# Kernel tuning notes

Measured on AMD Instinct MI355X. Metric: run time of the kernel, lower is better.

Reference implementation:

```python
import jax, jax.numpy as jnp
import numpy as np

N = 128            # codeword length (power of 2)
LIST = 8           # SCL list size
L2 = 2 * LIST      # decoders kept during path expansion
STAGES = 7         # log2(N)
LLR_MAX = 30.0
BATCH = 2048
FROZEN_POS = np.arange(N // 2)
FROZEN_IND = np.zeros(N, dtype=bool)
FROZEN_IND[FROZEN_POS] = True
INFO_POS = np.setdiff1d(np.arange(N), FROZEN_POS)


def _cn_op(x, y):
    # min-sum boxplus with LLR clipping
    x = jnp.clip(x, -LLR_MAX, LLR_MAX)
    y = jnp.clip(y, -LLR_MAX, LLR_MAX)
    return jnp.sign(x) * jnp.sign(y) * jnp.minimum(jnp.abs(x), jnp.abs(y))


def _vn_op(x, y, u):
    return (1.0 - 2.0 * u) * x + y


def _leaf(state, i):
    # Update single bit i across all 2L decoders, update path metrics,
    # and for info bits sort + duplicate the best L paths.
    uhat, llr, pm, ptr, bidx = state
    frozen = bool(FROZEN_IND[i])
    if not frozen:
        # set bit=1 for the upper half of decoders (path expansion)
        u_slice = uhat[:, :, 0, i]
        u_slice = u_slice.at[bidx[:, None], ptr[:, LIST:]].set(1.0)
        uhat = uhat.at[:, :, 0, i].set(u_slice)
    # path metric update, Eq.(10) of Stimming et al.
    u = jnp.take_along_axis(uhat[:, :, 0, i], ptr, axis=1)
    l = jnp.clip(jnp.take_along_axis(llr[:, :, 0, i], ptr, axis=1), -LLR_MAX, LLR_MAX)
    pm = pm + jax.nn.softplus(-(1.0 - 2.0 * u) * l)
    if not frozen:
        order = jnp.argsort(pm, axis=-1)
        pm = jnp.take_along_axis(pm, order, axis=1)
        ptr = jnp.take_along_axis(ptr, order, axis=1)
        lo = ptr[:, :LIST]
        up = ptr[:, LIST:]
        uhat = uhat.at[bidx[:, None], up].set(uhat[bidx[:, None], lo])
        llr = llr.at[bidx[:, None], up].set(llr[bidx[:, None], lo])
        pm = pm.at[:, LIST:].set(pm[:, :LIST])
    return (uhat, llr, pm, ptr, bidx)


def _decode(state, start, length):
    # recursive SCL tree traversal over contiguous index block [start, start+length)
    if length == 1:
        return _leaf(state, start)
    s = int(np.log2(length))
    h = length // 2
    uhat, llr, pm, ptr, bidx = state
    lsl = slice(start, start + h)
    rsl = slice(start + h, start + length)
    # f (check-node) update -> left child
    f = _cn_op(llr[:, :, s, lsl], llr[:, :, s, rsl])
    llr = llr.at[:, :, s - 1, lsl].set(f)
    uhat, llr, pm, ptr, bidx = _decode((uhat, llr, pm, ptr, bidx), start, h)
    # g (variable-node) update -> right child
    g = _vn_op(llr[:, :, s, lsl], llr[:, :, s, rsl], uhat[:, :, s - 1, lsl])
    llr = llr.at[:, :, s - 1, rsl].set(g)
    uhat, llr, pm, ptr, bidx = _decode((uhat, llr, pm, ptr, bidx), start + h, h)
    # combine partial sums: left XOR right, right pass-through
    ul = uhat[:, :, s - 1, lsl]
    ur = uhat[:, :, s - 1, rsl]
    ux = ul + ur - 2.0 * ul * ur  # XOR for {0,1} values (differentiable form)
    uhat = uhat.at[:, :, s, start:start + length].set(jnp.concatenate([ux, ur], axis=-1))
    return (uhat, llr, pm, ptr, bidx)


def setup_inputs() -> dict:
    key = jax.random.key(0)
    inputs = 2.0 * jax.random.normal(key, (BATCH, N), dtype=jnp.float32)
    return {"inputs": inputs}


def reference(inputs):
    bs = inputs.shape[0]
    llr_ch = -inputs.astype(jnp.float32)  # logits -> LLR sign convention
    uhat = jnp.zeros((bs, L2, STAGES + 1, N), jnp.float32)
    llr = jnp.zeros((bs, L2, STAGES + 1, N), jnp.float32)
    llr = llr.at[:, :, STAGES, :].set(llr_ch[:, None, :])
    pm = jnp.zeros((bs, L2), jnp.float32)
    pm = pm.at[:, 1:LIST].set(LLR_MAX).at[:, LIST + 1:].set(LLR_MAX)
    ptr = jnp.tile(jnp.arange(L2)[None, :], (bs, 1))
    bidx = jnp.arange(bs)
    uhat, llr, pm, ptr, _ = _decode((uhat, llr, pm, ptr, bidx), 0, N)
    # final sort and de-permutation of the list dimension
    order = jnp.argsort(pm, axis=-1)
    pm = jnp.take_along_axis(pm, order, axis=1)
    ptr = jnp.take_along_axis(ptr, order, axis=1)
    uhat = uhat[bidx[:, None], ptr]
    cand = jnp.argmin(pm, axis=-1)
    c_hat = uhat[bidx, cand, 0, :]       # [bs, n] best codeword estimate
    return c_hat[:, INFO_POS]            # [bs, k] info bits
```

## Files before the change

### kernel.cpp

```cpp
#include <hip/hip_runtime.h>
#include <math.h>

#define LMAX 30.0f
typedef unsigned long long ull;
typedef unsigned int u32;

__device__ __forceinline__ float clip30(float x) { return fminf(fmaxf(x, -LMAX), LMAX); }
__device__ __forceinline__ float cnop(float x, float y) {
    x = clip30(x); y = clip30(y);
    const float m = fminf(fabsf(x), fabsf(y));
    const unsigned sg = (__float_as_uint(x) ^ __float_as_uint(y)) & 0x80000000u;
    return __uint_as_float(__float_as_uint(m) | sg);
}

#define SWZI(x, PAT) __builtin_amdgcn_ds_swizzle((x), (PAT))
#define SWZF(x, PAT) __int_as_float(__builtin_amdgcn_ds_swizzle(__float_as_int(x), (PAT)))

template<int CTRL>
__device__ __forceinline__ int dppi(int x) {
    return __builtin_amdgcn_update_dpp(x, x, CTRL, 0xF, 0xF, false);
}
template<int CTRL>
__device__ __forceinline__ float dppf(float x) {
    return __int_as_float(dppi<CTRL>(__float_as_int(x)));
}
#define CTL_XOR8 0x128
#define CTL_XOR2 0x4E
#define CTL_XOR1 0xB1

#if __has_builtin(__builtin_amdgcn_permlane16_swap)
typedef int v2j_ __attribute__((ext_vector_type(2)));
__device__ __forceinline__ int swap16i(int x) {
    v2j_ r = __builtin_amdgcn_permlane16_swap(x, x, false, false);
    return (r[0] != x) ? r[0] : r[1];
}
#else
__device__ __forceinline__ int swap16i(int x) { return SWZI(x, 0x401F); }
#endif
__device__ __forceinline__ float swap16f(float x) { return __int_as_float(swap16i(__float_as_int(x))); }

__device__ __forceinline__ float gfb(float v, int a) {
    return __int_as_float(__builtin_amdgcn_ds_bpermute(a, __float_as_int(v)));
}
__device__ __forceinline__ u32 gub(u32 v, int a) {
    return (u32)__builtin_amdgcn_ds_bpermute(a, (int)v);
}

__device__ __forceinline__ u32 enc2(u32 w)  { w ^= (w >> 1) & 0x1u; return w; }
__device__ __forceinline__ u32 enc4(u32 w)  { w ^= (w >> 1) & 0x5u; w ^= (w >> 2) & 0x3u; return w; }
__device__ __forceinline__ u32 enc8(u32 w)  { w ^= (w >> 1) & 0x55u; w ^= (w >> 2) & 0x33u;
                                              w ^= (w >> 4) & 0x0fu; return w; }
__device__ __forceinline__ u32 enc16(u32 w) { w ^= (w >> 1) & 0x5555u; w ^= (w >> 2) & 0x3333u;
                                              w ^= (w >> 4) & 0x0f0fu; w ^= (w >> 8) & 0x00ffu; return w; }
__device__ __forceinline__ u32 enc32(u32 w) { w ^= (w >> 1) & 0x55555555u; w ^= (w >> 2) & 0x33333333u;
                                              w ^= (w >> 4) & 0x0f0f0f0fu; w ^= (w >> 8) & 0x00ff00ffu;
                                              w ^= (w >> 16) & 0x0000ffffu; return w; }

struct Dec {
    float C[32];
    float S5[16], S4[8], S3[4], R2[4], R1[2];
    float pm;
    u32 uhPrev, uhCur;
    int rF;
    int q, pos, gbase, A0, idx0;
    u32 upB;
    bool isUp;
};

__device__ __forceinline__ void f6(Dec& s) {
    #pragma unroll
    for (int k = 0; k < 16; ++k) s.S5[k] = cnop(s.C[k], s.C[k + 16]);
}
__device__ __forceinline__ void g6p(Dec& s) {
    const u32 ub = enc32(s.uhPrev);
    #pragma unroll
    for (int k = 0; k < 16; ++k) {
        const int u = (ub >> (s.q + 2 * k)) & 1;
        s.S5[k] = u ? (s.C[k + 16] - s.C[k]) : (s.C[k + 16] + s.C[k]);
    }
}
__device__ __forceinline__ void f5(Dec& s) {
    #pragma unroll
    for (int k = 0; k < 8; ++k) s.S4[k] = cnop(s.S5[k], s.S5[k + 8]);
}
template<int L> __device__ __forceinline__ void g5l(Dec& s) {
    const u32 ub = enc16((s.uhCur >> (L - 16)) & 0xffffu);
    #pragma unroll
    for (int k = 0; k < 8; ++k) {
        const int u = (ub >> (s.q + 2 * k)) & 1;
        s.S4[k] = u ? (s.S5[k + 8] - s.S5[k]) : (s.S5[k + 8] + s.S5[k]);
    }
}
__device__ __forceinline__ void f4(Dec& s) {
    #pragma unroll
    for (int k = 0; k < 4; ++k) s.S3[k] = cnop(s.S4[k], s.S4[k + 4]);
}
template<int L> __device__ __forceinline__ void g4l(Dec& s) {
    const u32 ub = enc8((s.uhCur >> (L - 8)) & 0xffu);
    #pragma unroll
    for (int k = 0; k < 4; ++k) {
        const int u = (ub >> (s.q + 2 * k)) & 1;
        s.S3[k] = u ? (s.S4[k + 4] - s.S4[k]) : (s.S4[k + 4] + s.S4[k]);
    }
}
__device__ __forceinline__ void repl2(Dec& s, float t0, float t1) {
    const float P0 = swap16f(t0), P1 = swap16f(t1);
    s.R2[0] = s.q ? P0 : t0; s.R2[1] = s.q ? t0 : P0;
    s.R2[2] = s.q ? P1 : t1; s.R2[3] = s.q ? t1 : P1;
}
__device__ __forceinline__ void f3r(Dec& s) {
    repl2(s, cnop(s.S3[0], s.S3[2]), cnop(s.S3[1], s.S3[3]));
}
template<int L> __device__ __forceinline__ void g3rl(Dec& s) {
    const u32 ub = enc4((s.uhCur >> (L - 4)) & 0xfu);
    const int u0 = (ub >> s.q) & 1, u1 = (ub >> (s.q + 2)) & 1;
    repl2(s, u0 ? (s.S3[2] - s.S3[0]) : (s.S3[2] + s.S3[0]),
             u1 ? (s.S3[3] - s.S3[1]) : (s.S3[3] + s.S3[1]));
}
__device__ __forceinline__ void f2(Dec& s) {
    s.R1[0] = cnop(s.R2[0], s.R2[2]); s.R1[1] = cnop(s.R2[1], s.R2[3]);
}
template<int L> __device__ __forceinline__ void g2l(Dec& s) {
    const u32 ub = enc2((s.uhCur >> (L - 2)) & 3u);
    s.R1[0] = (ub & 1) ? (s.R2[2] - s.R2[0]) : (s.R2[2] + s.R2[0]);
    s.R1[1] = (ub & 2) ? (s.R2[3] - s.R2[1]) : (s.R2[3] + s.R2[1]);
}

template<int L, int CLONEMODE>
__device__ __forceinline__ void leafR(Dec& s, float l0, int h) {
    s.uhCur |= s.upB << L;
    const float l = clip30(l0);
    const float tail = log1pf(expf(-fabsf(l)));
    s.pm += (s.isUp ? fmaxf(l, 0.0f) : fmaxf(-l, 0.0f)) + tail;
    int r = 0;
    {
        const u32 pmB = __float_as_uint(s.pm);
        #pragma unroll
        for (int k = 0; k < 8; ++k) {
            const u32 pmj = (u32)__builtin_amdgcn_ds_bpermute(s.A0 + 4 * k, __float_as_int(s.pm));
            r += ((pmj < pmB) || (pmj == pmB && (s.idx0 + k) < s.pos)) ? 1 : 0;
        }
    }
    r += swap16i(r);
    s.rF = r;
    if constexpr (CLONEMODE != 0) {
        if (CLONEMODE == 1 || h == 0) {
            const int inv = __builtin_amdgcn_ds_permute((r | s.gbase) << 2, s.pos);
            const int p8 = dppi<CTL_XOR8>(inv);
            const int ga = ((s.isUp ? p8 : inv) | s.gbase) << 2;
            s.pm = gfb(s.pm, ga);
            s.uhCur = gub(s.uhCur, ga);
            if (h != 0) s.uhPrev = gub(s.uhPrev, ga);
            if constexpr ((L & 1) == 0) {
                s.R1[0] = gfb(s.R1[0], ga); s.R1[1] = gfb(s.R1[1], ga);
            }
            if constexpr ((L & 2) == 0) {
                #pragma unroll
                for (int e = 0; e < 4; ++e) s.R2[e] = gfb(s.R2[e], ga);
            }
            if constexpr ((L & 4) == 0) {
                #pragma unroll
                for (int e = 0; e < 4; ++e) s.S3[e] = gfb(s.S3[e], ga);
            }
            if constexpr ((L & 8) == 0) {
                #pragma unroll
                for (int e = 0; e < 8; ++e) s.S4[e] = gfb(s.S4[e], ga);
            }
            if constexpr ((L & 16) == 0) {
                #pragma unroll
                for (int e = 0; e < 16; ++e) s.S5[e] = gfb(s.S5[e], ga);
            }
        }
    }
}

template<int J> __device__ __forceinline__ void evenL(Dec& s, int h) {
    constexpr int t = __builtin_ctz(J);
    if constexpr (t == 4) g5l<J>(s);
    if constexpr (t >= 4) f4(s);
    if constexpr (t == 3) g4l<J>(s);
    if constexpr (t >= 3) f3r(s);
    if constexpr (t == 2) g3rl<J>(s);
    if constexpr (t >= 2) f2(s);
    if constexpr (t == 1) g2l<J>(s);
    const float l0 = cnop(s.R1[0], s.R1[1]);
    leafR<J, 1>(s, l0, h);
}
template<int J> __device__ __forceinline__ void oddL(Dec& s, int h) {
    const int ug = (int)((s.uhCur >> (J - 1)) & 1u);
    const float l0 = ug ? (s.R1[1] - s.R1[0]) : (s.R1[1] + s.R1[0]);
    leafR<J, (J == 31 ? 2 : 1)>(s, l0, h);
}
template<int J> __device__ __forceinline__ void pairs(Dec& s, int h) {
    evenL<J>(s, h);
    oddL<J + 1>(s, h);
    if constexpr (J + 2 <= 30) pairs<J + 2>(s, h);
}

#define RLF(x, J) __uint_as_float((u32)__builtin_amdgcn_readlane(__float_as_int(x), (J)))

__global__ __launch_bounds__(64) void scl_kernel(const float* __restrict__ in,
                                                 float* __restrict__ out) {
    __shared__ float chS[128];
    const int lane = threadIdx.x;
    const int w = lane & 31;
    const int d = lane >> 5;
    const int dbase = lane & 32;

    Dec s;
    s.pos = lane & 15;
    s.q = (lane >> 4) & 1;
    s.gbase = lane & 48;
    s.isUp = (lane & 8) != 0;
    s.upB = (u32)((lane >> 3) & 1);
    s.idx0 = s.q << 3;
    s.A0 = (dbase | (s.q << 3)) << 2;
    s.uhPrev = 0; s.uhCur = 0; s.rF = 0;

    const size_t base = ((size_t)blockIdx.x * 2 + d) * 128;
    const float a1 = -in[base + w],      c1 = -in[base + 64 + w];
    const float a2 = -in[base + 32 + w], c2 = -in[base + 96 + w];
    chS[d * 64 + w] = a1 + c1;
    chS[d * 64 + 32 + w] = a2 + c2;
    __syncthreads();
    #pragma unroll
    for (int k = 0; k < 32; ++k) s.C[k] = chS[d * 64 + s.q + 2 * k];

    float v1 = cnop(a1, c1), v2 = cnop(a2, c2);
    { const float n1 = cnop(v1, v2); v2 = v1 + v2; v1 = n1; }
    { const float o1 = swap16f(v1), o2 = swap16f(v2);
      v1 = (w & 16) ? (o1 + v1) : cnop(v1, o1);
      v2 = (w & 16) ? (o2 + v2) : cnop(v2, o2); }
    { const float o1 = dppf<CTL_XOR8>(v1), o2 = dppf<CTL_XOR8>(v2);
      v1 = (w & 8) ? (o1 + v1) : cnop(v1, o1);
      v2 = (w & 8) ? (o2 + v2) : cnop(v2, o2); }
    { const float o1 = SWZF(v1, 0x101F), o2 = SWZF(v2, 0x101F);
      v1 = (w & 4) ? (o1 + v1) : cnop(v1, o1);
      v2 = (w & 4) ? (o2 + v2) : cnop(v2, o2); }
    { const float o1 = dppf<CTL_XOR2>(v1), o2 = dppf<CTL_XOR2>(v2);
      v1 = (w & 2) ? (o1 + v1) : cnop(v1, o1);
      v2 = (w & 2) ? (o2 + v2) : cnop(v2, o2); }
    { const float o1 = dppf<CTL_XOR1>(v1), o2 = dppf<CTL_XOR1>(v2);
      v1 = (w & 1) ? (o1 + v1) : cnop(v1, o1);
      v2 = (w & 1) ? (o2 + v2) : cnop(v2, o2); }
    const float sp1 = fmaxf(-clip30(v1), 0.0f) + log1pf(expf(-fabsf(clip30(v1))));
    const float sp2 = fmaxf(-clip30(v2), 0.0f) + log1pf(expf(-fabsf(clip30(v2))));

    s.pm = ((s.pos == 0) || (s.pos == 8)) ? 0.0f : LMAX;
    if (lane < 32) {
        #pragma unroll
        for (int j = 0; j < 32; ++j) s.pm += RLF(sp1, j);
        #pragma unroll
        for (int j = 0; j < 32; ++j) s.pm += RLF(sp2, j);
    } else {
        #pragma unroll
        for (int j = 32; j < 64; ++j) s.pm += RLF(sp1, j);
        #pragma unroll
        for (int j = 32; j < 64; ++j) s.pm += RLF(sp2, j);
    }

    #pragma unroll 1
    for (int h = 0; h < 2; ++h) {
        if (h == 0) f6(s); else g6p(s);
        f5(s); f4(s); f3r(s); f2(s);
        { const float l0 = cnop(s.R1[0], s.R1[1]); leafR<0, 1>(s, l0, h); }
        oddL<1>(s, h);
        pairs<2>(s, h);
        if (h == 0) { s.uhPrev = s.uhCur; s.uhCur = 0; }
    }

    const ull m = __ballot(s.rF == 0);
    const int bl = dbase + (int)__builtin_ctz((u32)(m >> dbase));
    const u32 b0 = gub(s.uhPrev, bl << 2);
    const u32 b1 = gub(s.uhCur, bl << 2);
    const size_t ob = ((size_t)blockIdx.x * 2 + d) * 64;
    out[ob + w] = (float)((b0 >> w) & 1u);
    out[ob + 32 + w] = (float)((b1 >> w) & 1u);
}

extern "C" void kernel_launch(void* const* d_in, const int* in_sizes, int n_in,
                              void* d_out, int out_size, void* d_ws, size_t ws_size,
                              hipStream_t stream) {
    (void)n_in; (void)out_size; (void)d_ws; (void)ws_size;
    const float* in = (const float*)d_in[0];
    float* out = (float*)d_out;
    const int batch = in_sizes[0] / 128;
    scl_kernel<<<dim3(batch / 2), dim3(64), 0, stream>>>(in, out);
}
```

Before: 52.90 us.

## Defer clone gathers of stage LLR buffers via per-stage source pointers

Instead of physically gathering the S3/S4/S5 LLR arrays across lanes on every clone step, each decoder now keeps a lane pointer per stage (mS3/mS4/mS5). Only that pointer is permuted when paths are duplicated, and the data is gathered lazily when the g-update reads the stage. The inverse-permutation computation is also changed from ds_permute plus a DPP swap to eight ballots followed by a bit-select and ctz. The intent is to cut the large number of ds_bpermute operations per info bit. The cost is extra bpermutes at g-update time and several ballots per leaf.

```diff
diff --git a/kernel.cpp b/kernel.cpp
--- a/kernel.cpp
+++ b/kernel.cpp
@@ -13,7 +13,6 @@
     return __uint_as_float(__float_as_uint(m) | sg);
 }
 
-#define SWZI(x, PAT) __builtin_amdgcn_ds_swizzle((x), (PAT))
 #define SWZF(x, PAT) __int_as_float(__builtin_amdgcn_ds_swizzle(__float_as_int(x), (PAT)))
 
 template<int CTRL>
@@ -35,7 +34,7 @@
     return (r[0] != x) ? r[0] : r[1];
 }
 #else
-__device__ __forceinline__ int swap16i(int x) { return SWZI(x, 0x401F); }
+__device__ __forceinline__ int swap16i(int x) { return __builtin_amdgcn_ds_swizzle(x, 0x401F); }
 #endif
 __device__ __forceinline__ float swap16f(float x) { return __int_as_float(swap16i(__float_as_int(x))); }
 
@@ -62,6 +61,7 @@
     float pm;
     u32 uhPrev, uhCur;
     int rF;
+    int mS5, mS4, mS3;
     int q, pos, gbase, A0, idx0;
     u32 upB;
     bool isUp;
@@ -83,13 +83,16 @@
     #pragma unroll
     for (int k = 0; k < 8; ++k) s.S4[k] = cnop(s.S5[k], s.S5[k + 8]);
 }
-template<int L> __device__ __forceinline__ void g5l(Dec& s) {
-    const u32 ub = enc16((s.uhCur >> (L - 16)) & 0xffffu);
+__device__ __forceinline__ void g5l16(Dec& s) {
+    const u32 ub = enc16(s.uhCur & 0xffffu);
+    const int am = (s.mS5 | s.gbase) << 2;
     #pragma unroll
     for (int k = 0; k < 8; ++k) {
+        const float x = gfb(s.S5[k], am), y = gfb(s.S5[k + 8], am);
         const int u = (ub >> (s.q + 2 * k)) & 1;
-        s.S4[k] = u ? (s.S5[k + 8] - s.S5[k]) : (s.S5[k + 8] + s.S5[k]);
-    }
+        s.S4[k] = u ? (y - x) : (y + x);
+    }
+    s.mS4 = s.pos;
 }
 __device__ __forceinline__ void f4(Dec& s) {
     #pragma unroll
@@ -97,11 +100,14 @@
 }
 template<int L> __device__ __forceinline__ void g4l(Dec& s) {
     const u32 ub = enc8((s.uhCur >> (L - 8)) & 0xffu);
+    const int am = (s.mS4 | s.gbase) << 2;
     #pragma unroll
     for (int k = 0; k < 4; ++k) {
+        const float x = gfb(s.S4[k], am), y = gfb(s.S4[k + 4], am);
         const int u = (ub >> (s.q + 2 * k)) & 1;
-        s.S3[k] = u ? (s.S4[k + 4] - s.S4[k]) : (s.S4[k + 4] + s.S4[k]);
-    }
+        s.S3[k] = u ? (y - x) : (y + x);
+    }
+    s.mS3 = s.pos;
 }
 __device__ __forceinline__ void repl2(Dec& s, float t0, float t1) {
     const float P0 = swap16f(t0), P1 = swap16f(t1);
@@ -113,9 +119,11 @@
 }
 template<int L> __device__ __forceinline__ void g3rl(Dec& s) {
     const u32 ub = enc4((s.uhCur >> (L - 4)) & 0xfu);
+    const int am = (s.mS3 | s.gbase) << 2;
+    const float x0 = gfb(s.S3[0], am), x1 = gfb(s.S3[1], am);
+    const float x2 = gfb(s.S3[2], am), x3 = gfb(s.S3[3], am);
     const int u0 = (ub >> s.q) & 1, u1 = (ub >> (s.q + 2)) & 1;
-    repl2(s, u0 ? (s.S3[2] - s.S3[0]) : (s.S3[2] + s.S3[0]),
-             u1 ? (s.S3[3] - s.S3[1]) : (s.S3[3] + s.S3[1]));
+    repl2(s, u0 ? (x2 - x0) : (x2 + x0), u1 ? (x3 - x1) : (x3 + x1));
 }
 __device__ __forceinline__ void f2(Dec& s) {
     s.R1[0] = cnop(s.R2[0], s.R2[2]); s.R1[1] = cnop(s.R2[1], s.R2[3]);
@@ -145,9 +153,19 @@
     s.rF = r;
     if constexpr (CLONEMODE != 0) {
         if (CLONEMODE == 1 || h == 0) {
-            const int inv = __builtin_amdgcn_ds_permute((r | s.gbase) << 2, s.pos);
-            const int p8 = dppi<CTL_XOR8>(inv);
-            const int ga = ((s.isUp ? p8 : inv) | s.gbase) << 2;
+            const ull b0 = __ballot(r == 0), b1 = __ballot(r == 1);
+            const ull b2 = __ballot(r == 2), b3 = __ballot(r == 3);
+            const ull b4 = __ballot(r == 4), b5 = __ballot(r == 5);
+            const ull b6 = __ballot(r == 6), b7 = __ballot(r == 7);
+            const ull t0 = (s.pos & 1) ? b1 : b0;
+            const ull t1 = (s.pos & 1) ? b3 : b2;
+            const ull t2 = (s.pos & 1) ? b5 : b4;
+            const ull t3 = (s.pos & 1) ? b7 : b6;
+            const ull u0 = (s.pos & 2) ? t1 : t0;
+            const ull u1 = (s.pos & 2) ? t3 : t2;
+            const ull bb = (s.pos & 4) ? u1 : u0;
+            const u32 win = (u32)(bb >> s.gbase) & 0xFFFFu;
+            const int ga = (((int)__builtin_ctz(win)) | s.gbase) << 2;
             s.pm = gfb(s.pm, ga);
             s.uhCur = gub(s.uhCur, ga);
             if (h != 0) s.uhPrev = gub(s.uhPrev, ga);
@@ -158,31 +176,21 @@
                 #pragma unroll
                 for (int e = 0; e < 4; ++e) s.R2[e] = gfb(s.R2[e], ga);
             }
-            if constexpr ((L & 4) == 0) {
-                #pragma unroll
-                for (int e = 0; e < 4; ++e) s.S3[e] = gfb(s.S3[e], ga);
-            }
-            if constexpr ((L & 8) == 0) {
-                #pragma unroll
-                for (int e = 0; e < 8; ++e) s.S4[e] = gfb(s.S4[e], ga);
-            }
-            if constexpr ((L & 16) == 0) {
-                #pragma unroll
-                for (int e = 0; e < 16; ++e) s.S5[e] = gfb(s.S5[e], ga);
-            }
+            if constexpr ((L & 4) == 0) s.mS3 = __builtin_amdgcn_ds_bpermute(ga, s.mS3);
+            if constexpr ((L & 8) == 0) s.mS4 = __builtin_amdgcn_ds_bpermute(ga, s.mS4);
+            if constexpr ((L & 16) == 0) s.mS5 = __builtin_amdgcn_ds_bpermute(ga, s.mS5);
         }
     }
 }
 
 template<int J> __device__ __forceinline__ void evenL(Dec& s, int h) {
     constexpr int t = __builtin_ctz(J);
-    if constexpr (t == 4) g5l<J>(s);
-    if constexpr (t >= 4) f4(s);
-    if constexpr (t == 3) g4l<J>(s);
-    if constexpr (t >= 3) f3r(s);
-    if constexpr (t == 2) g3rl<J>(s);
-    if constexpr (t >= 2) f2(s);
-    if constexpr (t == 1) g2l<J>(s);
+    if constexpr (t == 4) { g5l16(s); f4(s); s.mS3 = s.pos; }
+    if constexpr (t == 3) { g4l<J>(s); }
+    if constexpr (t >= 3) { f3r(s); }
+    if constexpr (t == 2) { g3rl<J>(s); }
+    if constexpr (t >= 2) { f2(s); }
+    if constexpr (t == 1) { g2l<J>(s); }
     const float l0 = cnop(s.R1[0], s.R1[1]);
     leafR<J, 1>(s, l0, h);
 }
@@ -262,7 +270,10 @@
     #pragma unroll 1
     for (int h = 0; h < 2; ++h) {
         if (h == 0) f6(s); else g6p(s);
-        f5(s); f4(s); f3r(s); f2(s);
+        s.mS5 = s.pos;
+        f5(s); s.mS4 = s.pos;
+        f4(s); s.mS3 = s.pos;
+        f3r(s); f2(s);
         { const float l0 = cnop(s.R1[0], s.R1[1]); leafR<0, 1>(s, l0, h); }
         oddL<1>(s, h);
         pairs<2>(s, h);
```

Measured after the change: 51.89 us. No clear change (-1.9%).
